# Performance work log

Measured on AMD Instinct MI355X. Metric: run time of the kernel, lower is better.

## Reference

```python
import jax, jax.numpy as jnp
import numpy as np

_SAMPLING_EPS = 1e-5


def setup_inputs() -> dict:
    key = jax.random.key(0)
    k1, k2, k3, k4, k5, k6 = jax.random.split(key, 6)
    B, V = 128, 128000
    return {
        "logits": jax.random.normal(k1, (B, V), dtype=jnp.float32),
        "temperature": jax.random.uniform(k2, (B,), dtype=jnp.float32),
        "min_p": jax.random.uniform(k3, (B,), dtype=jnp.float32),
        "top_k": jax.random.randint(k4, (B,), 0, 1024),
        "top_p": jax.random.uniform(k5, (B,), dtype=jnp.float32),
        "q": jax.random.uniform(k6, (B, V), dtype=jnp.float32),
        "num_logprobs": 20,
    }


def reference(logits, temperature, min_p, top_k, top_p, q, num_logprobs):
    B, V = logits.shape
    # raw logprobs computed BEFORE any processing (as in Sampler.forward)
    raw_logprobs = jax.nn.log_softmax(logits, axis=-1)
    # greedy sample on unscaled logits
    greedy = jnp.argmax(logits, axis=-1)
    # temperature scaling
    lt = logits / temperature[:, None]
    # min-p filtering
    probs = jax.nn.softmax(lt, axis=-1)
    max_p = jnp.max(probs, axis=-1, keepdims=True)
    lt = jnp.where(probs >= min_p[:, None] * max_p, lt, -jnp.inf)
    # top-k / top-p filtering on ascending-sorted logits (vLLM style)
    idx = jnp.argsort(lt, axis=-1)                       # ascending
    ls = jnp.take_along_axis(lt, idx, axis=-1)
    k = jnp.clip(top_k, 1, V)
    kth = jnp.take_along_axis(ls, (V - k)[:, None], axis=-1)  # k-th largest value
    ls = jnp.where(ls < kth, -jnp.inf, ls)
    ps = jax.nn.softmax(ls, axis=-1)
    csum = jnp.cumsum(ps, axis=-1)
    pmask = csum <= (1.0 - top_p)[:, None]
    pmask = pmask.at[:, -1].set(False)                   # always keep the max token
    ls = jnp.where(pmask, -jnp.inf, ls)
    inv = jnp.argsort(idx, axis=-1)                      # inverse permutation (scatter back)
    filtered = jnp.take_along_axis(ls, inv, axis=-1)
    # exponential-race sampling: argmax(probs / Exp(1)) ~ Categorical(probs)
    probs2 = jax.nn.softmax(filtered, axis=-1)
    expo = -jnp.log(jnp.clip(q, 1e-10, 1.0))
    rand_sampled = jnp.argmax(probs2 / expo, axis=-1)
    sampled = jnp.where(temperature < _SAMPLING_EPS, greedy, rand_sampled)
    # gather_logprobs: top-k logprobs + sampled-token logprob + rank
    topk_lp, topk_idx = jax.lax.top_k(raw_logprobs, num_logprobs)
    tok_lp = jnp.take_along_axis(raw_logprobs, sampled[:, None], axis=-1)  # (B,1)
    ranks = jnp.sum(raw_logprobs >= tok_lp, axis=-1)
    out_idx = jnp.concatenate([sampled[:, None], topk_idx], axis=1).astype(jnp.int32)
    out_lp = jnp.concatenate([tok_lp, topk_lp], axis=1)  # (B, num_logprobs+1)
    return (sampled[:, None].astype(jnp.int32), out_idx, out_lp, ranks)
```

## Files before the change

kernel.cpp:

```cpp
#include <hip/hip_runtime.h>
#include <math.h>

#define S_CHUNKS 16
#define NB 1024
#define C_CAP 2048
#define BLKA 256
#define BLK2 512
#define LCAP2 512
#define FLOORB 682
#define BIN_SCALE ((float)NB / 12.0f)

__device__ __forceinline__ int bin_of(float x) {
  int b = (int)floorf((x + 6.0f) * BIN_SCALE);
  return min(max(b, 0), NB - 1);
}
__device__ __forceinline__ unsigned long long pack_vi(float v, int idx) {
  return ((unsigned long long)__float_as_uint(v) << 32) | (unsigned int)idx;
}
__device__ __forceinline__ unsigned long long okey(float v, int idx) {
  unsigned int u = __float_as_uint(v);
  u = (u & 0x80000000u) ? ~u : (u | 0x80000000u);
  return ((unsigned long long)u << 32) | (unsigned long long)(0x7fffffffu - (unsigned int)idx);
}
__device__ __forceinline__ float okey_val(unsigned long long k) {
  unsigned int hi = (unsigned int)(k >> 32);
  unsigned int u = (hi & 0x80000000u) ? (hi & 0x7fffffffu) : ~hi;
  return __uint_as_float(u);
}
__device__ __forceinline__ int okey_idx(unsigned long long k) {
  return (int)(0x7fffffffu - (unsigned int)k);
}

__global__ __launch_bounds__(BLKA)
void kA_hist(const float* __restrict__ logits, int V, int chunkElems,
             unsigned short* __restrict__ chist, float* __restrict__ psum,
             unsigned long long* __restrict__ plist, int* __restrict__ pcnt) {
  const int row = blockIdx.y, chunk = blockIdx.x, tid = threadIdx.x;
  const float* lrow = logits + (size_t)row * V;
  const int start = chunk * chunkElems;
  const int end = min(start + chunkElems, V);
  __shared__ unsigned int hist[NB];
  __shared__ unsigned long long lst[LCAP2];
  __shared__ float rs[BLKA];
  __shared__ int lcnt;
  for (int i = tid; i < NB; i += BLKA) hist[i] = 0u;
  if (tid == 0) lcnt = 0;
  __syncthreads();
  float sum = 0.0f;
  const int n = max(end - start, 0);
  const int n4 = n >> 2;
  const float4* p4 = (const float4*)(lrow + start);
  int i = tid;
  for (; i + BLKA < n4; i += 2 * BLKA) {
    float4 a = p4[i], b2 = p4[i + BLKA];
    float va[8] = {a.x, a.y, a.z, a.w, b2.x, b2.y, b2.z, b2.w};
    int ia[8];
    #pragma unroll
    for (int c = 0; c < 4; c++) { ia[c] = start + (i << 2) + c; ia[c + 4] = start + ((i + BLKA) << 2) + c; }
    #pragma unroll
    for (int c = 0; c < 8; c++) {
      float x = va[c];
      int b = bin_of(x);
      atomicAdd(&hist[b], 1u);
      sum += __expf(fminf(x, 70.0f) - 6.0f);
      if (b >= FLOORB) {
        int p = atomicAdd(&lcnt, 1);
        if (p < LCAP2) lst[p] = pack_vi(x, ia[c]);
      }
    }
  }
  for (; i < n4; i += BLKA) {
    float4 a = p4[i];
    float va[4] = {a.x, a.y, a.z, a.w};
    #pragma unroll
    for (int c = 0; c < 4; c++) {
      float x = va[c];
      int b = bin_of(x);
      atomicAdd(&hist[b], 1u);
      sum += __expf(fminf(x, 70.0f) - 6.0f);
      if (b >= FLOORB) {
        int p = atomicAdd(&lcnt, 1);
        if (p < LCAP2) lst[p] = pack_vi(x, start + (i << 2) + c);
      }
    }
  }
  for (int j = (n4 << 2) + tid; j < n; j += BLKA) {
    float x = lrow[start + j];
    int b = bin_of(x);
    atomicAdd(&hist[b], 1u);
    sum += __expf(fminf(x, 70.0f) - 6.0f);
    if (b >= FLOORB) {
      int p = atomicAdd(&lcnt, 1);
      if (p < LCAP2) lst[p] = pack_vi(x, start + j);
    }
  }
  __syncthreads();
  rs[tid] = sum;
  __syncthreads();
  for (int s = BLKA / 2; s > 0; s >>= 1) {
    if (tid < s) rs[tid] += rs[tid + s];
    __syncthreads();
  }
  const size_t rc = (size_t)row * S_CHUNKS + chunk;
  if (tid == 0) { psum[rc] = rs[0]; pcnt[rc] = lcnt; }
  unsigned short* hrow = chist + rc * NB;
  for (int j = tid; j < NB; j += BLKA)
    hrow[j] = (unsigned short)min(hist[j], 65535u);
  int m = min(lcnt, LCAP2);
  unsigned long long* prow = plist + rc * LCAP2;
  for (int j = tid; j < m; j += BLKA) prow[j] = lst[j];
}

__global__ __launch_bounds__(BLK2)
void k2_fused(const float* __restrict__ logits,
              const float* __restrict__ temperature,
              const float* __restrict__ min_p,
              const int* __restrict__ top_k,
              const float* __restrict__ top_p,
              const float* __restrict__ q,
              const int* __restrict__ nl_ptr,
              int V, int B, int chunkElems,
              const unsigned short* __restrict__ chist,
              const float* __restrict__ psum,
              const unsigned long long* __restrict__ plist,
              const int* __restrict__ pcnt,
              float* __restrict__ out) {
  const int row = blockIdx.x, tid = threadIdx.x;
  __shared__ int h[NB + 1];
  __shared__ int cur[NB];
  __shared__ unsigned long long bkt[C_CAP];
  __shared__ float sv[C_CAP];
  __shared__ int   si[C_CAP];
  __shared__ float ss[C_CAP];
  __shared__ float st[BLK2], rf[BLK2], rf2[BLK2];
  __shared__ int   ri[BLK2];
  __shared__ int   s_fail, s_b, s_m;
  __shared__ float s_lse;

  #pragma unroll
  for (int k = 0; k < NB / BLK2; k++) {
    int i = tid + k * BLK2;
    int s = 0;
    for (int c = 0; c < S_CHUNKS; c++)
      s += chist[((size_t)row * S_CHUNKS + c) * NB + i];
    h[i] = s;
    cur[i] = 0;
  }
  if (tid == 0) { h[NB] = 0; s_b = 0; s_m = 0; s_fail = 0; }
  __syncthreads();
  if (tid < S_CHUNKS) atomicMax(&s_m, pcnt[(size_t)row * S_CHUNKS + tid]);
  for (int off = 1; off < NB; off <<= 1) {
    int t0[NB / BLK2];
    #pragma unroll
    for (int k = 0; k < NB / BLK2; k++) {
      int i = tid + k * BLK2;
      t0[k] = (i + off < NB) ? h[i + off] : 0;
    }
    __syncthreads();
    #pragma unroll
    for (int k = 0; k < NB / BLK2; k++) h[tid + k * BLK2] += t0[k];
    __syncthreads();
  }
  int nl = nl_ptr[0];
  int ke = top_k[row]; ke = min(max(ke, 1), V);
  int Kp = max(ke, nl);
  #pragma unroll
  for (int k = 0; k < NB / BLK2; k++) {
    int i = tid + k * BLK2;
    if (h[i] >= Kp) atomicMax(&s_b, i);
  }
  if (tid == 0) {
    float t = 0.0f;
    for (int c = 0; c < S_CHUNKS; c++) t += psum[(size_t)row * S_CHUNKS + c];
    s_lse = 6.0f + logf(t);
  }
  __syncthreads();
  const int bstar = s_b;
  const bool fast = (bstar >= FLOORB && s_m <= LCAP2);
  int c = min(h[bstar], C_CAP); if (c < 1) c = 1;

  if (fast) {
    for (int chunk = 0; chunk < S_CHUNKS; chunk++) {
      const size_t rc = (size_t)row * S_CHUNKS + chunk;
      const int m = pcnt[rc];
      const unsigned long long* prow = plist + rc * LCAP2;
      for (int j = tid; j < m; j += BLK2) {
        unsigned long long kk = prow[j];
        float x = __uint_as_float((unsigned int)(kk >> 32));
        int idx = (int)(unsigned int)kk;
        int b = bin_of(x);
        if (b >= bstar) {
          int a = atomicAdd(&cur[b], 1);
          int pos = h[b + 1] + a;
          if (pos < C_CAP) bkt[pos] = okey(x, idx);
        }
      }
    }
  } else {
    const float* lrow = logits + (size_t)row * V;
    const int n4 = V >> 2;
    const float4* p4 = (const float4*)lrow;
    for (int i = tid; i < n4; i += BLK2) {
      float4 a4 = p4[i];
      float va[4] = {a4.x, a4.y, a4.z, a4.w};
      #pragma unroll
      for (int cc = 0; cc < 4; cc++) {
        int b = bin_of(va[cc]);
        if (b >= bstar) {
          int a = atomicAdd(&cur[b], 1);
          int pos = h[b + 1] + a;
          if (pos < C_CAP) bkt[pos] = okey(va[cc], (i << 2) + cc);
        }
      }
    }
    for (int j = (n4 << 2) + tid; j < V; j += BLK2) {
      float x = lrow[j];
      int b = bin_of(x);
      if (b >= bstar) {
        int a = atomicAdd(&cur[b], 1);
        int pos = h[b + 1] + a;
        if (pos < C_CAP) bkt[pos] = okey(x, j);
      }
    }
  }
  __syncthreads();
  for (int pos = tid; pos < c; pos += BLK2) {
    unsigned long long k0 = bkt[pos];
    float v = okey_val(k0);
    int b = bin_of(v);
    int gs = h[b + 1];
    int ge = min(h[b], c);
    int rk = 0;
    for (int j = gs; j < ge; j++) if (bkt[j] > k0) rk++;
    int fin = gs + rk;
    sv[fin] = v; si[fin] = okey_idx(k0);
  }
  __syncthreads();

  float temp = temperature[row];
  bool ug = (temp < 1e-5f);
  float rt = 1.0f / (ug ? 1.0f : temp);
  float mp = min_p[row], tp = top_p[row];
  ke = min(ke, c);
  float v0 = sv[0];
  float lt0 = v0 * rt;

  float ltk = sv[ke - 1] * rt;
  float kth = (expf(ltk - lt0) >= mp) ? ltk : -INFINITY;

  if (tid == 0) s_fail = c;
  __syncthreads();
  for (int i = tid; i < c; i += BLK2) {
    float ltj = sv[i] * rt;
    if (!((expf(ltj - lt0) >= mp) && (ltj >= kth))) { atomicMin(&s_fail, i); break; }
  }
  __syncthreads();
  int n1 = s_fail; if (n1 < 1) n1 = 1;
  __syncthreads();

  int L = (c + BLK2 - 1) / BLK2;
  int base = tid * L;
  int lim = min(base + L, c);
  float run = 0.0f;
  for (int j = base; j < lim; j++) {
    float pj = (j < n1) ? expf(sv[j] * rt - lt0) : 0.0f;
    run += pj; ss[j] = run;
  }
  st[tid] = run;
  __syncthreads();
  for (int off = 1; off < BLK2; off <<= 1) {
    float t0 = (tid >= off) ? st[tid - off] : 0.0f;
    __syncthreads();
    st[tid] += t0;
    __syncthreads();
  }
  float offv = (tid > 0) ? st[tid - 1] : 0.0f;
  for (int j = base; j < lim; j++) ss[j] += offv;
  __syncthreads();
  float Z1 = ss[n1 - 1];

  if (tid == 0) s_fail = n1;
  __syncthreads();
  for (int i = tid; i < n1; i += BLK2) {
    if (i > 0 && !((1.0f - ss[i - 1] / Z1) > (1.0f - tp))) { atomicMin(&s_fail, i); break; }
  }
  __syncthreads();
  int n2 = s_fail; if (n2 < 1) n2 = 1;
  __syncthreads();
  float Z2 = ss[n2 - 1];

  const float* qrow = q + (size_t)row * V;
  float bsc = -INFINITY; int bidx = 0x7fffffff; float bval = 0.0f;
  for (int i = tid; i < n2; i += BLK2) {
    float pj = expf(sv[i] * rt - lt0);
    float qv = qrow[si[i]];
    qv = fminf(fmaxf(qv, 1e-10f), 1.0f);
    float sc = (pj / Z2) / (-logf(qv));
    if (sc > bsc || (sc == bsc && si[i] < bidx)) { bsc = sc; bidx = si[i]; bval = sv[i]; }
  }
  rf[tid] = bsc; ri[tid] = bidx; rf2[tid] = bval;
  __syncthreads();
  for (int s = BLK2 / 2; s > 0; s >>= 1) {
    if (tid < s) {
      if (rf[tid + s] > rf[tid] ||
          (rf[tid + s] == rf[tid] && ri[tid + s] < ri[tid])) {
        rf[tid] = rf[tid + s]; ri[tid] = ri[tid + s]; rf2[tid] = rf2[tid + s];
      }
    }
    __syncthreads();
  }
  int sampled = ug ? si[0] : ri[0];
  float val_s = ug ? sv[0] : rf2[0];
  float lse = s_lse;
  float tok_lp = val_s - lse;
  __syncthreads();

  if (tid == 0) s_fail = c;
  __syncthreads();
  for (int i = tid; i < c; i += BLK2)
    if (!((sv[i] - lse) >= tok_lp)) { atomicMin(&s_fail, i); break; }
  __syncthreads();
  int rank = s_fail;

  int W = nl + 1;
  if (tid == 0) {
    out[row] = (float)sampled;
    out[B + row * W] = (float)sampled;
    out[B + B * W + row * W] = tok_lp;
    out[B + 2 * B * W + row] = (float)rank;
  }
  for (int t = tid; t < nl; t += BLK2) {
    out[B + row * W + 1 + t] = (float)si[t];
    out[B + B * W + row * W + 1 + t] = sv[t] - lse;
  }
}

extern "C" void kernel_launch(void* const* d_in, const int* in_sizes, int n_in,
                              void* d_out, int out_size, void* d_ws, size_t ws_size,
                              hipStream_t stream) {
  const float* logits      = (const float*)d_in[0];
  const float* temperature = (const float*)d_in[1];
  const float* min_p       = (const float*)d_in[2];
  const int*   top_k       = (const int*)d_in[3];
  const float* top_p       = (const float*)d_in[4];
  const float* q           = (const float*)d_in[5];
  const int*   nl_ptr      = (const int*)d_in[6];

  int B = in_sizes[1];
  int V = in_sizes[0] / B;
  float* out = (float*)d_out;
  int chunkElems = ((V + S_CHUNKS - 1) / S_CHUNKS + 3) & ~3;

  unsigned char* w = (unsigned char*)d_ws;
  unsigned long long* plist = (unsigned long long*)w; w += (size_t)B * S_CHUNKS * LCAP2 * sizeof(unsigned long long);
  unsigned short* chist = (unsigned short*)w;         w += (size_t)B * S_CHUNKS * NB * sizeof(unsigned short);
  float* psum = (float*)w;                            w += (size_t)B * S_CHUNKS * sizeof(float);
  int* pcnt = (int*)w;                                w += (size_t)B * S_CHUNKS * sizeof(int);

  hipLaunchKernelGGL(kA_hist, dim3(S_CHUNKS, B), dim3(BLKA), 0, stream,
                     logits, V, chunkElems, chist, psum, plist, pcnt);
  hipLaunchKernelGGL(k2_fused, dim3(B), dim3(BLK2), 0, stream,
                     logits, temperature, min_p, top_k, top_p, q, nl_ptr,
                     V, B, chunkElems, chist, psum, plist, pcnt, out);
}
```

Baseline: 175.6 us.

## Fuse histogram pass and selection kernel into single per-row kernel

Merges the chunked histogram/prefilter kernel into the selection kernel so each row is handled by one 1024-thread block that builds the histogram, log-sum-exp and candidate list in shared memory. This removes the second launch and the global workspace round-trip of per-chunk histograms and candidate lists. In exchange the whole grid shrinks to one block per row, so fewer compute units share the streaming pass and its shared-memory atomics, and shared-memory use per block grows.

```diff
diff --git a/kernel.cpp b/kernel.cpp
--- a/kernel.cpp
+++ b/kernel.cpp
@@ -1,12 +1,10 @@
 #include <hip/hip_runtime.h>
 #include <math.h>
 
-#define S_CHUNKS 16
 #define NB 1024
 #define C_CAP 2048
-#define BLKA 256
-#define BLK2 512
-#define LCAP2 512
+#define BLK 1024
+#define PRECAP 4096
 #define FLOORB 682
 #define BIN_SCALE ((float)NB / 12.0f)
 
@@ -31,189 +29,136 @@
   return (int)(0x7fffffffu - (unsigned int)k);
 }
 
-__global__ __launch_bounds__(BLKA)
-void kA_hist(const float* __restrict__ logits, int V, int chunkElems,
-             unsigned short* __restrict__ chist, float* __restrict__ psum,
-             unsigned long long* __restrict__ plist, int* __restrict__ pcnt) {
-  const int row = blockIdx.y, chunk = blockIdx.x, tid = threadIdx.x;
-  const float* lrow = logits + (size_t)row * V;
-  const int start = chunk * chunkElems;
-  const int end = min(start + chunkElems, V);
-  __shared__ unsigned int hist[NB];
-  __shared__ unsigned long long lst[LCAP2];
-  __shared__ float rs[BLKA];
-  __shared__ int lcnt;
-  for (int i = tid; i < NB; i += BLKA) hist[i] = 0u;
-  if (tid == 0) lcnt = 0;
-  __syncthreads();
-  float sum = 0.0f;
-  const int n = max(end - start, 0);
-  const int n4 = n >> 2;
-  const float4* p4 = (const float4*)(lrow + start);
-  int i = tid;
-  for (; i + BLKA < n4; i += 2 * BLKA) {
-    float4 a = p4[i], b2 = p4[i + BLKA];
-    float va[8] = {a.x, a.y, a.z, a.w, b2.x, b2.y, b2.z, b2.w};
-    int ia[8];
-    #pragma unroll
-    for (int c = 0; c < 4; c++) { ia[c] = start + (i << 2) + c; ia[c + 4] = start + ((i + BLKA) << 2) + c; }
-    #pragma unroll
-    for (int c = 0; c < 8; c++) {
-      float x = va[c];
-      int b = bin_of(x);
-      atomicAdd(&hist[b], 1u);
-      sum += __expf(fminf(x, 70.0f) - 6.0f);
-      if (b >= FLOORB) {
-        int p = atomicAdd(&lcnt, 1);
-        if (p < LCAP2) lst[p] = pack_vi(x, ia[c]);
-      }
-    }
-  }
-  for (; i < n4; i += BLKA) {
-    float4 a = p4[i];
-    float va[4] = {a.x, a.y, a.z, a.w};
-    #pragma unroll
-    for (int c = 0; c < 4; c++) {
-      float x = va[c];
-      int b = bin_of(x);
-      atomicAdd(&hist[b], 1u);
-      sum += __expf(fminf(x, 70.0f) - 6.0f);
-      if (b >= FLOORB) {
-        int p = atomicAdd(&lcnt, 1);
-        if (p < LCAP2) lst[p] = pack_vi(x, start + (i << 2) + c);
-      }
-    }
-  }
-  for (int j = (n4 << 2) + tid; j < n; j += BLKA) {
-    float x = lrow[start + j];
-    int b = bin_of(x);
-    atomicAdd(&hist[b], 1u);
-    sum += __expf(fminf(x, 70.0f) - 6.0f);
-    if (b >= FLOORB) {
-      int p = atomicAdd(&lcnt, 1);
-      if (p < LCAP2) lst[p] = pack_vi(x, start + j);
-    }
-  }
-  __syncthreads();
-  rs[tid] = sum;
-  __syncthreads();
-  for (int s = BLKA / 2; s > 0; s >>= 1) {
-    if (tid < s) rs[tid] += rs[tid + s];
-    __syncthreads();
-  }
-  const size_t rc = (size_t)row * S_CHUNKS + chunk;
-  if (tid == 0) { psum[rc] = rs[0]; pcnt[rc] = lcnt; }
-  unsigned short* hrow = chist + rc * NB;
-  for (int j = tid; j < NB; j += BLKA)
-    hrow[j] = (unsigned short)min(hist[j], 65535u);
-  int m = min(lcnt, LCAP2);
-  unsigned long long* prow = plist + rc * LCAP2;
-  for (int j = tid; j < m; j += BLKA) prow[j] = lst[j];
-}
-
-__global__ __launch_bounds__(BLK2)
-void k2_fused(const float* __restrict__ logits,
-              const float* __restrict__ temperature,
-              const float* __restrict__ min_p,
-              const int* __restrict__ top_k,
-              const float* __restrict__ top_p,
-              const float* __restrict__ q,
-              const int* __restrict__ nl_ptr,
-              int V, int B, int chunkElems,
-              const unsigned short* __restrict__ chist,
-              const float* __restrict__ psum,
-              const unsigned long long* __restrict__ plist,
-              const int* __restrict__ pcnt,
-              float* __restrict__ out) {
+__global__ __launch_bounds__(BLK)
+void sampler_fused(const float* __restrict__ logits,
+                   const float* __restrict__ temperature,
+                   const float* __restrict__ min_p,
+                   const int* __restrict__ top_k,
+                   const float* __restrict__ top_p,
+                   const float* __restrict__ q,
+                   const int* __restrict__ nl_ptr,
+                   int V, int B,
+                   float* __restrict__ out) {
   const int row = blockIdx.x, tid = threadIdx.x;
   __shared__ int h[NB + 1];
   __shared__ int cur[NB];
+  __shared__ unsigned long long lst[PRECAP];
   __shared__ unsigned long long bkt[C_CAP];
   __shared__ float sv[C_CAP];
   __shared__ int   si[C_CAP];
   __shared__ float ss[C_CAP];
-  __shared__ float st[BLK2], rf[BLK2], rf2[BLK2];
-  __shared__ int   ri[BLK2];
-  __shared__ int   s_fail, s_b, s_m;
+  __shared__ float st[BLK];
+  __shared__ float rf[BLK], rf2[BLK];
+  __shared__ int   ri[BLK];
+  __shared__ int   s_fail, s_b, s_cnt;
   __shared__ float s_lse;
 
-  #pragma unroll
-  for (int k = 0; k < NB / BLK2; k++) {
-    int i = tid + k * BLK2;
-    int s = 0;
-    for (int c = 0; c < S_CHUNKS; c++)
-      s += chist[((size_t)row * S_CHUNKS + c) * NB + i];
-    h[i] = s;
-    cur[i] = 0;
-  }
-  if (tid == 0) { h[NB] = 0; s_b = 0; s_m = 0; s_fail = 0; }
-  __syncthreads();
-  if (tid < S_CHUNKS) atomicMax(&s_m, pcnt[(size_t)row * S_CHUNKS + tid]);
+  for (int i = tid; i < NB; i += BLK) { h[i] = 0; cur[i] = 0; }
+  if (tid == 0) { s_b = 0; s_cnt = 0; h[NB] = 0; }
+  __syncthreads();
+
+  const float* lrow = logits + (size_t)row * V;
+  float sum = 0.0f;
+  const int n4 = V >> 2;
+  const float4* p4 = (const float4*)lrow;
+  int i = tid;
+  for (; i + BLK < n4; i += 2 * BLK) {
+    float4 a = p4[i], b2 = p4[i + BLK];
+    float va[8] = {a.x, a.y, a.z, a.w, b2.x, b2.y, b2.z, b2.w};
+    int ia[8];
+    #pragma unroll
+    for (int c2 = 0; c2 < 4; c2++) { ia[c2] = (i << 2) + c2; ia[c2 + 4] = ((i + BLK) << 2) + c2; }
+    #pragma unroll
+    for (int c2 = 0; c2 < 8; c2++) {
+      float x = va[c2];
+      int b = bin_of(x);
+      atomicAdd(&h[b], 1);
+      sum += __expf(fminf(x, 70.0f) - 6.0f);
+      if (b >= FLOORB) {
+        int p = atomicAdd(&s_cnt, 1);
+        if (p < PRECAP) lst[p] = pack_vi(x, ia[c2]);
+      }
+    }
+  }
+  for (; i < n4; i += BLK) {
+    float4 a = p4[i];
+    float va[4] = {a.x, a.y, a.z, a.w};
+    #pragma unroll
+    for (int c2 = 0; c2 < 4; c2++) {
+      float x = va[c2];
+      int b = bin_of(x);
+      atomicAdd(&h[b], 1);
+      sum += __expf(fminf(x, 70.0f) - 6.0f);
+      if (b >= FLOORB) {
+        int p = atomicAdd(&s_cnt, 1);
+        if (p < PRECAP) lst[p] = pack_vi(x, (i << 2) + c2);
+      }
+    }
+  }
+  for (int j = (n4 << 2) + tid; j < V; j += BLK) {
+    float x = lrow[j];
+    int b = bin_of(x);
+    atomicAdd(&h[b], 1);
+    sum += __expf(fminf(x, 70.0f) - 6.0f);
+    if (b >= FLOORB) {
+      int p = atomicAdd(&s_cnt, 1);
+      if (p < PRECAP) lst[p] = pack_vi(x, j);
+    }
+  }
+  __syncthreads();
+
+  st[tid] = sum;
+  __syncthreads();
+  for (int s = BLK / 2; s > 0; s >>= 1) {
+    if (tid < s) st[tid] += st[tid + s];
+    __syncthreads();
+  }
+  if (tid == 0) s_lse = 6.0f + logf(st[0]);
+
   for (int off = 1; off < NB; off <<= 1) {
-    int t0[NB / BLK2];
-    #pragma unroll
-    for (int k = 0; k < NB / BLK2; k++) {
-      int i = tid + k * BLK2;
-      t0[k] = (i + off < NB) ? h[i + off] : 0;
-    }
-    __syncthreads();
-    #pragma unroll
-    for (int k = 0; k < NB / BLK2; k++) h[tid + k * BLK2] += t0[k];
+    int t0 = (tid + off < NB) ? h[tid + off] : 0;
+    __syncthreads();
+    h[tid] += t0;
     __syncthreads();
   }
   int nl = nl_ptr[0];
   int ke = top_k[row]; ke = min(max(ke, 1), V);
   int Kp = max(ke, nl);
-  #pragma unroll
-  for (int k = 0; k < NB / BLK2; k++) {
-    int i = tid + k * BLK2;
-    if (h[i] >= Kp) atomicMax(&s_b, i);
-  }
-  if (tid == 0) {
-    float t = 0.0f;
-    for (int c = 0; c < S_CHUNKS; c++) t += psum[(size_t)row * S_CHUNKS + c];
-    s_lse = 6.0f + logf(t);
-  }
+  if (h[tid] >= Kp) atomicMax(&s_b, tid);
   __syncthreads();
   const int bstar = s_b;
-  const bool fast = (bstar >= FLOORB && s_m <= LCAP2);
+  const int total_pre = s_cnt;
+  const bool fast = (bstar >= FLOORB) && (total_pre <= PRECAP);
   int c = min(h[bstar], C_CAP); if (c < 1) c = 1;
 
   if (fast) {
-    for (int chunk = 0; chunk < S_CHUNKS; chunk++) {
-      const size_t rc = (size_t)row * S_CHUNKS + chunk;
-      const int m = pcnt[rc];
-      const unsigned long long* prow = plist + rc * LCAP2;
-      for (int j = tid; j < m; j += BLK2) {
-        unsigned long long kk = prow[j];
-        float x = __uint_as_float((unsigned int)(kk >> 32));
-        int idx = (int)(unsigned int)kk;
-        int b = bin_of(x);
+    int m = min(total_pre, PRECAP);
+    for (int j = tid; j < m; j += BLK) {
+      unsigned long long kk = lst[j];
+      float x = __uint_as_float((unsigned int)(kk >> 32));
+      int idx = (int)(unsigned int)kk;
+      int b = bin_of(x);
+      if (b >= bstar) {
+        int a = atomicAdd(&cur[b], 1);
+        int pos = h[b + 1] + a;
+        if (pos < C_CAP) bkt[pos] = okey(x, idx);
+      }
+    }
+  } else {
+    for (int ii = tid; ii < n4; ii += BLK) {
+      float4 a4 = p4[ii];
+      float va[4] = {a4.x, a4.y, a4.z, a4.w};
+      #pragma unroll
+      for (int c2 = 0; c2 < 4; c2++) {
+        int b = bin_of(va[c2]);
         if (b >= bstar) {
           int a = atomicAdd(&cur[b], 1);
           int pos = h[b + 1] + a;
-          if (pos < C_CAP) bkt[pos] = okey(x, idx);
+          if (pos < C_CAP) bkt[pos] = okey(va[c2], (ii << 2) + c2);
         }
       }
     }
-  } else {
-    const float* lrow = logits + (size_t)row * V;
-    const int n4 = V >> 2;
-    const float4* p4 = (const float4*)lrow;
-    for (int i = tid; i < n4; i += BLK2) {
-      float4 a4 = p4[i];
-      float va[4] = {a4.x, a4.y, a4.z, a4.w};
-      #pragma unroll
-      for (int cc = 0; cc < 4; cc++) {
-        int b = bin_of(va[cc]);
-        if (b >= bstar) {
-          int a = atomicAdd(&cur[b], 1);
-          int pos = h[b + 1] + a;
-          if (pos < C_CAP) bkt[pos] = okey(va[cc], (i << 2) + cc);
-        }
-      }
-    }
-    for (int j = (n4 << 2) + tid; j < V; j += BLK2) {
+    for (int j = (n4 << 2) + tid; j < V; j += BLK) {
       float x = lrow[j];
       int b = bin_of(x);
       if (b >= bstar) {
@@ -224,7 +169,8 @@
     }
   }
   __syncthreads();
-  for (int pos = tid; pos < c; pos += BLK2) {
+
+  for (int pos = tid; pos < c; pos += BLK) {
     unsigned long long k0 = bkt[pos];
     float v = okey_val(k0);
     int b = bin_of(v);
@@ -250,15 +196,15 @@
 
   if (tid == 0) s_fail = c;
   __syncthreads();
-  for (int i = tid; i < c; i += BLK2) {
-    float ltj = sv[i] * rt;
-    if (!((expf(ltj - lt0) >= mp) && (ltj >= kth))) { atomicMin(&s_fail, i); break; }
+  for (int ii = tid; ii < c; ii += BLK) {
+    float ltj = sv[ii] * rt;
+    if (!((expf(ltj - lt0) >= mp) && (ltj >= kth))) { atomicMin(&s_fail, ii); break; }
   }
   __syncthreads();
   int n1 = s_fail; if (n1 < 1) n1 = 1;
   __syncthreads();
 
-  int L = (c + BLK2 - 1) / BLK2;
+  int L = (c + BLK - 1) / BLK;
   int base = tid * L;
   int lim = min(base + L, c);
   float run = 0.0f;
@@ -268,7 +214,7 @@
   }
   st[tid] = run;
   __syncthreads();
-  for (int off = 1; off < BLK2; off <<= 1) {
+  for (int off = 1; off < BLK; off <<= 1) {
     float t0 = (tid >= off) ? st[tid - off] : 0.0f;
     __syncthreads();
     st[tid] += t0;
@@ -281,8 +227,8 @@
 
   if (tid == 0) s_fail = n1;
   __syncthreads();
-  for (int i = tid; i < n1; i += BLK2) {
-    if (i > 0 && !((1.0f - ss[i - 1] / Z1) > (1.0f - tp))) { atomicMin(&s_fail, i); break; }
+  for (int ii = tid; ii < n1; ii += BLK) {
+    if (ii > 0 && !((1.0f - ss[ii - 1] / Z1) > (1.0f - tp))) { atomicMin(&s_fail, ii); break; }
   }
   __syncthreads();
   int n2 = s_fail; if (n2 < 1) n2 = 1;
@@ -291,16 +237,16 @@
 
   const float* qrow = q + (size_t)row * V;
   float bsc = -INFINITY; int bidx = 0x7fffffff; float bval = 0.0f;
-  for (int i = tid; i < n2; i += BLK2) {
-    float pj = expf(sv[i] * rt - lt0);
-    float qv = qrow[si[i]];
+  for (int ii = tid; ii < n2; ii += BLK) {
+    float pj = expf(sv[ii] * rt - lt0);
+    float qv = qrow[si[ii]];
     qv = fminf(fmaxf(qv, 1e-10f), 1.0f);
     float sc = (pj / Z2) / (-logf(qv));
-    if (sc > bsc || (sc == bsc && si[i] < bidx)) { bsc = sc; bidx = si[i]; bval = sv[i]; }
+    if (sc > bsc || (sc == bsc && si[ii] < bidx)) { bsc = sc; bidx = si[ii]; bval = sv[ii]; }
   }
   rf[tid] = bsc; ri[tid] = bidx; rf2[tid] = bval;
   __syncthreads();
-  for (int s = BLK2 / 2; s > 0; s >>= 1) {
+  for (int s = BLK / 2; s > 0; s >>= 1) {
     if (tid < s) {
       if (rf[tid + s] > rf[tid] ||
           (rf[tid + s] == rf[tid] && ri[tid + s] < ri[tid])) {
@@ -317,8 +263,8 @@
 
   if (tid == 0) s_fail = c;
   __syncthreads();
-  for (int i = tid; i < c; i += BLK2)
-    if (!((sv[i] - lse) >= tok_lp)) { atomicMin(&s_fail, i); break; }
+  for (int ii = tid; ii < c; ii += BLK)
+    if (!((sv[ii] - lse) >= tok_lp)) { atomicMin(&s_fail, ii); break; }
   __syncthreads();
   int rank = s_fail;
 
@@ -329,7 +275,7 @@
     out[B + B * W + row * W] = tok_lp;
     out[B + 2 * B * W + row] = (float)rank;
   }
-  for (int t = tid; t < nl; t += BLK2) {
+  for (int t = tid; t < nl; t += BLK) {
     out[B + row * W + 1 + t] = (float)si[t];
     out[B + B * W + row * W + 1 + t] = sv[t] - lse;
   }
@@ -349,17 +295,8 @@
   int B = in_sizes[1];
   int V = in_sizes[0] / B;
   float* out = (float*)d_out;
-  int chunkElems = ((V + S_CHUNKS - 1) / S_CHUNKS + 3) & ~3;
-
-  unsigned char* w = (unsigned char*)d_ws;
-  unsigned long long* plist = (unsigned long long*)w; w += (size_t)B * S_CHUNKS * LCAP2 * sizeof(unsigned long long);
-  unsigned short* chist = (unsigned short*)w;         w += (size_t)B * S_CHUNKS * NB * sizeof(unsigned short);
-  float* psum = (float*)w;                            w += (size_t)B * S_CHUNKS * sizeof(float);
-  int* pcnt = (int*)w;                                w += (size_t)B * S_CHUNKS * sizeof(int);
-
-  hipLaunchKernelGGL(kA_hist, dim3(S_CHUNKS, B), dim3(BLKA), 0, stream,
-                     logits, V, chunkElems, chist, psum, plist, pcnt);
-  hipLaunchKernelGGL(k2_fused, dim3(B), dim3(BLK2), 0, stream,
+
+  hipLaunchKernelGGL(sampler_fused, dim3(B), dim3(BLK), 0, stream,
                      logits, temperature, min_p, top_k, top_p, q, nl_ptr,
-                     V, B, chunkElems, chist, psum, plist, pcnt, out);
-}
+                     V, B, out);
+}
```

Result: faster. 167.2 us (-4.8%).
